# Performance work log

Measured on AMD Instinct MI355X. Metric: run time of the kernel, lower is better.

## Reference

```python
import jax, jax.numpy as jnp
import numpy as np

B_SZ, SEQ, D_IN = 8, 4096, 1024
STATE, HEADS = 1024, 16
HEAD_DIM = STATE // HEADS
LN_EPS = 1e-5


def setup_inputs() -> dict:
    key = jax.random.key(0)
    ks = jax.random.split(key, 10)
    inp = {
        "x": jax.random.normal(ks[0], (B_SZ, SEQ, D_IN), dtype=jnp.float32),
        "W_in": jax.random.normal(ks[1], (STATE, D_IN), dtype=jnp.float32) * (1.0 / np.sqrt(D_IN)),
        "b_in": jnp.zeros((STATE,), dtype=jnp.float32),
        "log_A": jax.random.normal(ks[2], (HEADS, HEAD_DIM), dtype=jnp.float32) * 0.1 + 0.1,
        "B_p": jax.random.normal(ks[3], (HEADS, HEAD_DIM), dtype=jnp.float32) * 0.1 + 0.1,
        "C_p": jax.random.normal(ks[4], (HEADS, HEAD_DIM), dtype=jnp.float32) * 0.1 + 0.1,
        "W_out": jax.random.normal(ks[5], (STATE, STATE), dtype=jnp.float32) * (1.0 / np.sqrt(STATE)),
        "b_out": jnp.zeros((STATE,), dtype=jnp.float32),
        "gamma": jnp.ones((STATE,), dtype=jnp.float32),
        "beta": jnp.zeros((STATE,), dtype=jnp.float32),
    }
    return inp


def reference(x, W_in, b_in, log_A, B_p, C_p, W_out, b_out, gamma, beta):
    Bsz, S, _ = x.shape
    H, Dh = log_A.shape
    # input projection: (B,S,state)
    h = jnp.einsum("bsd,ed->bse", x, W_in) + b_in
    h = h.reshape(Bsz, S, H, Dh)
    decay = jnp.exp(-jax.nn.softplus(log_A))  # (H,Dh), time-invariant

    def step(s, xt):  # s,xt: (B,H,Dh)
        s = s * decay + B_p * xt
        return s, C_p * s

    s0 = jnp.zeros((Bsz, H, Dh), dtype=h.dtype)
    _, ys = jax.lax.scan(step, s0, jnp.swapaxes(h, 0, 1))  # ys: (S,B,H,Dh)
    y = jnp.swapaxes(ys, 0, 1).reshape(Bsz, S, H * Dh)
    out = jnp.einsum("bse,fe->bsf", y, W_out) + b_out
    # dropout in eval mode = identity; layer norm over last dim
    mu = out.mean(-1, keepdims=True)
    var = out.var(-1, keepdims=True)
    return (out - mu) * jax.lax.rsqrt(var + LN_EPS) * gamma + beta
```

## Files before the change

### kernel.cpp

```cpp
#include <hip/hip_runtime.h>

#define B_SZ  8
#define SEQ   4096
#define D_IN  1024
#define STATE 1024
#define M_TOT (B_SZ * SEQ)
#define LN_EPS 1e-5f
#define GK    1024
#define GN    1024

#define SCAN_L 64
#define SCAN_W 64

typedef short short8_t __attribute__((ext_vector_type(8)));
typedef float f32x4 __attribute__((ext_vector_type(4)));

__device__ __forceinline__ unsigned short f2bf(float f) {
  union { float f; unsigned u; } v; v.f = f;
  unsigned r = v.u + 0x7fffu + ((v.u >> 16) & 1u);
  return (unsigned short)(r >> 16);
}
__device__ __forceinline__ float bf2f(unsigned short h) {
  union { unsigned u; float f; } v; v.u = ((unsigned)h) << 16;
  return v.f;
}

__device__ __forceinline__ void gload16(const void* g, void* l) {
  __builtin_amdgcn_global_load_lds(
      (const __attribute__((address_space(1))) void*)g,
      (__attribute__((address_space(3))) void*)l, 16, 0, 0);
}

#define BAR()    __builtin_amdgcn_s_barrier()
#define SCHED0() __builtin_amdgcn_sched_barrier(0)

__global__ __launch_bounds__(256) void cast_kernel(const float* __restrict__ in,
                                                   unsigned short* __restrict__ out,
                                                   int n4) {
  const int stride = gridDim.x * 256;
  for (int i = blockIdx.x * 256 + threadIdx.x; i < n4; i += stride) {
    float4 v = ((const float4*)in)[i];
    ushort4 o;
    o.x = f2bf(v.x); o.y = f2bf(v.y); o.z = f2bf(v.z); o.w = f2bf(v.w);
    ((ushort4*)out)[i] = o;
  }
}

__global__ __launch_bounds__(256) void cast2_kernel(const float* __restrict__ a,
                                                    const float* __restrict__ b,
                                                    unsigned short* __restrict__ oa,
                                                    unsigned short* __restrict__ ob,
                                                    int n4each) {
  const int stride = gridDim.x * 256;
  for (int i = blockIdx.x * 256 + threadIdx.x; i < 2 * n4each; i += stride) {
    const bool second = (i >= n4each);
    const int j = second ? i - n4each : i;
    float4 v = second ? ((const float4*)b)[j] : ((const float4*)a)[j];
    ushort4 o;
    o.x = f2bf(v.x); o.y = f2bf(v.y); o.z = f2bf(v.z); o.w = f2bf(v.w);
    if (second) ((ushort4*)ob)[j] = o; else ((ushort4*)oa)[j] = o;
  }
}

__device__ __forceinline__ void stageA(const char* g, char* d, int t) {
  gload16(g + t * 64, d);
}
__device__ __forceinline__ void stageB(const char* g, char* d, int t, int h) {
  gload16(g + h * (128 * (long)GK * 2) + t * 64, d + h * 8192);
}

template <int H>
__device__ __forceinline__ void readA(const char* pk, short8_t (&a)[2]) {
#pragma unroll
  for (int mf = 0; mf < 2; mf++)
    a[mf] = *(const short8_t*)(pk + H * 2048 + mf * 1024);
}
template <int NH>
__device__ __forceinline__ void readB(const char* pk, short8_t (&b)[2]) {
#pragma unroll
  for (int nf = 0; nf < 2; nf++)
    b[nf] = *(const short8_t*)(pk + NH * 2048 + nf * 1024);
}

template <int H, int NH>
__device__ __forceinline__ void mfma4(short8_t (&a)[2], short8_t (&b)[2],
                                      f32x4 (&acc)[4][4]) {
  __builtin_amdgcn_s_setprio(1);
#pragma unroll
  for (int mf = 0; mf < 2; mf++)
#pragma unroll
    for (int nf = 0; nf < 2; nf++)
      acc[H * 2 + mf][NH * 2 + nf] = __builtin_amdgcn_mfma_f32_16x16x32_bf16(
          a[mf], b[nf], acc[H * 2 + mf][NH * 2 + nf], 0, 0, 0);
  __builtin_amdgcn_s_setprio(0);
}

__global__ __launch_bounds__(512, 4) void gemm128(
    const unsigned short* __restrict__ A,
    const unsigned short* __restrict__ Bt,
    const float* __restrict__ bias,
    unsigned short* __restrict__ C,
    int M) {
  __shared__ __attribute__((aligned(16))) unsigned short As[2][128 * 32];
  __shared__ __attribute__((aligned(16))) unsigned short Bs[2][256 * 32];

  const int tid = threadIdx.x;
  const int w = tid >> 6, lane = tid & 63;
  const int wm = w >> 2, wn = w & 3;
  const int fr = lane & 15;
  const int fkb = (lane >> 4) * 16;

  const int nwg = gridDim.x;
  const int cpx = nwg >> 3;
  const int bid = blockIdx.x;
  const int wg = (bid & 7) * cpx + (bid >> 3);
  const int nbx = GN >> 8;
  const long m0 = (long)(wg / nbx) * 128;
  const long n0 = (long)(wg % nbx) * 256;

  const int ko = fkb ^ (((fr >> 1) & 3) << 4);
  const int rb = fr * 64 + ko;
  const char* pA0 = (const char*)&As[0][0] + wm * 4096 + rb;
  const char* pA1 = (const char*)&As[1][0] + wm * 4096 + rb;
  const char* pB0 = (const char*)&Bs[0][0] + wn * 4096 + rb;
  const char* pB1 = (const char*)&Bs[1][0] + wn * 4096 + rb;

  const int srow = tid >> 2;
  const int c2 = ((tid & 3) * 16) ^ (((srow >> 1) & 3) << 4);
  const char* gA0 = (const char*)(A  + (m0 + srow) * (long)GK) + c2;
  const char* gB0 = (const char*)(Bt + (n0 + srow) * (long)GK) + c2;
  char* dA0 = (char*)&As[0][0] + ((tid >> 6) << 10);
  char* dA1 = (char*)&As[1][0] + ((tid >> 6) << 10);
  char* dB0 = (char*)&Bs[0][0] + ((tid >> 6) << 10);
  char* dB1 = (char*)&Bs[1][0] + ((tid >> 6) << 10);

  short8_t aE[2], aO[2], b0[2], b1[2];
  f32x4 acc[4][4] = {};

  const int nit = (GK / 32) >> 1;

  stageA(gA0, dA0, 0);
  stageB(gB0, dB0, 0, 0);
  stageB(gB0, dB0, 0, 1);
  SCHED0();
  asm volatile("s_waitcnt vmcnt(0)" ::: "memory");
  BAR();

#pragma unroll 1
  for (int i = 0; i < nit; ++i) {
    const bool last = (i == nit - 1);
    const int t1 = 2 * i + 1, t2 = 2 * i + 2;

    readA<0>(pA0, aE);
    readB<0>(pB0, b0);
    stageA(gA0, dA1, t1);
    SCHED0(); BAR();
    mfma4<0, 0>(aE, b0, acc);
    SCHED0(); BAR();

    readB<1>(pB0, b1);
    stageB(gB0, dB1, t1, 0);
    stageB(gB0, dB1, t1, 1);
    SCHED0(); BAR();
    mfma4<0, 1>(aE, b1, acc);
    SCHED0(); BAR();

    readA<1>(pA0, aO);
    SCHED0(); BAR();
    mfma4<1, 0>(aO, b0, acc);
    SCHED0(); BAR();

    SCHED0(); BAR();
    mfma4<1, 1>(aO, b1, acc);
    SCHED0();
    asm volatile("s_waitcnt vmcnt(0)" ::: "memory");
    BAR();

    readA<0>(pA1, aE);
    readB<0>(pB1, b0);
    if (!last) stageA(gA0, dA0, t2);
    SCHED0(); BAR();
    mfma4<0, 0>(aE, b0, acc);
    SCHED0(); BAR();

    readB<1>(pB1, b1);
    if (!last) {
      stageB(gB0, dB0, t2, 0);
      stageB(gB0, dB0, t2, 1);
    }
    SCHED0(); BAR();
    mfma4<0, 1>(aE, b1, acc);
    SCHED0(); BAR();

    readA<1>(pA1, aO);
    SCHED0(); BAR();
    mfma4<1, 0>(aO, b0, acc);
    SCHED0(); BAR();

    SCHED0(); BAR();
    mfma4<1, 1>(aO, b1, acc);
    SCHED0();
    if (!last) { asm volatile("s_waitcnt vmcnt(0)" ::: "memory"); }
    BAR();
  }

  const int cc = lane & 15;
  const int cr = (lane >> 4) * 4;
  char* epi = (w < 4) ? ((char*)&As[0][0] + w * 4096)
                      : ((char*)&Bs[0][0] + (w - 4) * 4096);
  float bv[4];
#pragma unroll
  for (int nf = 0; nf < 4; nf++) bv[nf] = bias[n0 + wn * 64 + nf * 16 + cc];
  const int rr = lane >> 3;
  const int rdo = rr * 128 + (((lane & 7) * 16) ^ ((rr & 7) << 4));
#pragma unroll
  for (int half = 0; half < 2; ++half) {
#pragma unroll
    for (int m2 = 0; m2 < 2; ++m2) {
      const int mf = half * 2 + m2;
#pragma unroll
      for (int r = 0; r < 4; ++r) {
        const int rowc = m2 * 16 + cr + r;
        const int rx = (rowc & 7) << 4;
#pragma unroll
        for (int nf = 0; nf < 4; ++nf) {
          const int off = rowc * 128 + (((nf * 16 + cc) * 2) ^ rx);
          *(unsigned short*)(epi + off) = f2bf(acc[mf][nf][r] + bv[nf]);
        }
      }
    }
    char* cb = (char*)C + (m0 + wm * 64 + half * 32) * (GN * 2)
             + (n0 + wn * 64) * 2 + (lane & 7) * 16;
#pragma unroll
    for (int s = 0; s < 4; ++s) {
      short8_t vv = *(const short8_t*)(epi + s * 1024 + rdo);
      *(short8_t*)(cb + (long)(s * 8 + rr) * (GN * 2)) = vv;
    }
  }
}

__global__ __launch_bounds__(256) void scan_kernel(
    const unsigned short* __restrict__ h,
    const float* __restrict__ log_A,
    const float* __restrict__ Bp,
    const float* __restrict__ Cp,
    unsigned short* __restrict__ y) {
  const int e0 = threadIdx.x * 4;
  const int chunk = blockIdx.x;
  const int b = blockIdx.y;
  const float4 la = *(const float4*)&log_A[e0];
  const float4 bp = *(const float4*)&Bp[e0];
  const float4 cp = *(const float4*)&Cp[e0];
  float d[4], bpv[4], cpv[4];
  d[0] = expf(-log1pf(expf(la.x))); d[1] = expf(-log1pf(expf(la.y)));
  d[2] = expf(-log1pf(expf(la.z))); d[3] = expf(-log1pf(expf(la.w)));
  bpv[0] = bp.x; bpv[1] = bp.y; bpv[2] = bp.z; bpv[3] = bp.w;
  cpv[0] = cp.x; cpv[1] = cp.y; cpv[2] = cp.z; cpv[3] = cp.w;

  const long base = ((long)b * SEQ) * STATE + e0;
  const int t0 = chunk * SCAN_L;
  const int tw = (t0 >= SCAN_W) ? (t0 - SCAN_W) : 0;
  float s[4] = {0.f, 0.f, 0.f, 0.f};

  for (int t = tw; t < t0; ++t) {
    ushort4 hv = *(const ushort4*)&h[base + (long)t * STATE];
    s[0] = fmaf(s[0], d[0], bpv[0] * bf2f(hv.x));
    s[1] = fmaf(s[1], d[1], bpv[1] * bf2f(hv.y));
    s[2] = fmaf(s[2], d[2], bpv[2] * bf2f(hv.z));
    s[3] = fmaf(s[3], d[3], bpv[3] * bf2f(hv.w));
  }
  for (int t = t0; t < t0 + SCAN_L; ++t) {
    ushort4 hv = *(const ushort4*)&h[base + (long)t * STATE];
    s[0] = fmaf(s[0], d[0], bpv[0] * bf2f(hv.x));
    s[1] = fmaf(s[1], d[1], bpv[1] * bf2f(hv.y));
    s[2] = fmaf(s[2], d[2], bpv[2] * bf2f(hv.z));
    s[3] = fmaf(s[3], d[3], bpv[3] * bf2f(hv.w));
    ushort4 o;
    o.x = f2bf(cpv[0] * s[0]); o.y = f2bf(cpv[1] * s[1]);
    o.z = f2bf(cpv[2] * s[2]); o.w = f2bf(cpv[3] * s[3]);
    *(ushort4*)&y[base + (long)t * STATE] = o;
  }
}

__global__ __launch_bounds__(128) void ln_kernel(
    const unsigned short* __restrict__ X,
    const float* __restrict__ gamma,
    const float* __restrict__ beta,
    float* __restrict__ out) {
  const int row = blockIdx.x;
  const int tid = threadIdx.x;
  const long base = (long)row * STATE;
  short8_t v = *(const short8_t*)&X[base + tid * 8];
  float x[8];
#pragma unroll
  for (int j = 0; j < 8; j++) x[j] = bf2f((unsigned short)v[j]);
  float s = 0.f, q = 0.f;
#pragma unroll
  for (int j = 0; j < 8; j++) { s += x[j]; q += x[j] * x[j]; }
#pragma unroll
  for (int o = 32; o > 0; o >>= 1) {
    s += __shfl_xor(s, o);
    q += __shfl_xor(q, o);
  }
  __shared__ float sw[2], qw[2];
  const int wave = tid >> 6, lane = tid & 63;
  if (lane == 0) { sw[wave] = s; qw[wave] = q; }
  __syncthreads();
  s = sw[0] + sw[1];
  q = qw[0] + qw[1];
  const float mu = s * (1.0f / STATE);
  const float var = q * (1.0f / STATE) - mu * mu;
  const float inv = rsqrtf(var + LN_EPS);
  const int c = tid * 8;
  float4 g0 = *(const float4*)&gamma[c], g1 = *(const float4*)&gamma[c + 4];
  float4 be0 = *(const float4*)&beta[c], be1 = *(const float4*)&beta[c + 4];
  float4 o0, o1;
  o0.x = (x[0] - mu) * inv * g0.x + be0.x;
  o0.y = (x[1] - mu) * inv * g0.y + be0.y;
  o0.z = (x[2] - mu) * inv * g0.z + be0.z;
  o0.w = (x[3] - mu) * inv * g0.w + be0.w;
  o1.x = (x[4] - mu) * inv * g1.x + be1.x;
  o1.y = (x[5] - mu) * inv * g1.y + be1.y;
  o1.z = (x[6] - mu) * inv * g1.z + be1.z;
  o1.w = (x[7] - mu) * inv * g1.w + be1.w;
  *(float4*)&out[base + c] = o0;
  *(float4*)&out[base + c + 4] = o1;
}

extern "C" void kernel_launch(void* const* d_in, const int* in_sizes, int n_in,
                              void* d_out, int out_size, void* d_ws, size_t ws_size,
                              hipStream_t stream) {
  const float* x     = (const float*)d_in[0];
  const float* W_in  = (const float*)d_in[1];
  const float* b_in  = (const float*)d_in[2];
  const float* log_A = (const float*)d_in[3];
  const float* Bp    = (const float*)d_in[4];
  const float* Cp    = (const float*)d_in[5];
  const float* W_out = (const float*)d_in[6];
  const float* b_out = (const float*)d_in[7];
  const float* gamma = (const float*)d_in[8];
  const float* beta  = (const float*)d_in[9];
  float* out = (float*)d_out;

  char* ws = (char*)d_ws;
  unsigned short* Wi_b = (unsigned short*)(ws);
  unsigned short* Wo_b = (unsigned short*)(ws + (2ull << 20));
  unsigned short* xb   = (unsigned short*)(ws + (4ull << 20));
  unsigned short* hb   = (unsigned short*)(ws + (68ull << 20));

  cast_kernel<<<4096, 256, 0, stream>>>(x, xb, M_TOT * D_IN / 4);
  cast2_kernel<<<2048, 256, 0, stream>>>(W_in, W_out, Wi_b, Wo_b, STATE * D_IN / 4);

  gemm128<<<dim3((GN / 256) * (M_TOT / 128)), 512, 0, stream>>>(
      xb, Wi_b, b_in, hb, M_TOT);

  scan_kernel<<<dim3(SEQ / SCAN_L, B_SZ), 256, 0, stream>>>(
      hb, log_A, Bp, Cp, xb);

  gemm128<<<dim3((GN / 256) * (M_TOT / 128)), 512, 0, stream>>>(
      xb, Wo_b, b_out, hb, M_TOT);

  ln_kernel<<<M_TOT, 128, 0, stream>>>(hb, gamma, beta, out);
}
```

Measured before the change: 256.7 us.

## Fuse fp32-to-bf16 cast of x into the input-projection GEMM

Removes the standalone cast kernel for x and adds a GEMM variant that stages fp32 x tiles straight into LDS, converting them to bf16 when reading MFMA fragments. This avoids writing and re-reading the 64MB bf16 copy of x. In exchange the A tile in LDS doubles to fp32, which raises LDS use per block and may reduce occupancy, and every fragment read now does extra conversion work.

```diff
diff --git a/kernel.cpp b/kernel.cpp
--- a/kernel.cpp
+++ b/kernel.cpp
@@ -1,4 +1,5 @@
 #include <hip/hip_runtime.h>
+#include <hip/hip_bf16.h>
 
 #define B_SZ  8
 #define SEQ   4096
@@ -33,18 +34,6 @@
 
 #define BAR()    __builtin_amdgcn_s_barrier()
 #define SCHED0() __builtin_amdgcn_sched_barrier(0)
-
-__global__ __launch_bounds__(256) void cast_kernel(const float* __restrict__ in,
-                                                   unsigned short* __restrict__ out,
-                                                   int n4) {
-  const int stride = gridDim.x * 256;
-  for (int i = blockIdx.x * 256 + threadIdx.x; i < n4; i += stride) {
-    float4 v = ((const float4*)in)[i];
-    ushort4 o;
-    o.x = f2bf(v.x); o.y = f2bf(v.y); o.z = f2bf(v.z); o.w = f2bf(v.w);
-    ((ushort4*)out)[i] = o;
-  }
-}
 
 __global__ __launch_bounds__(256) void cast2_kernel(const float* __restrict__ a,
                                                     const float* __restrict__ b,
@@ -62,11 +51,8 @@
   }
 }
 
-__device__ __forceinline__ void stageA(const char* g, char* d, int t) {
-  gload16(g + t * 64, d);
-}
-__device__ __forceinline__ void stageB(const char* g, char* d, int t, int h) {
-  gload16(g + h * (128 * (long)GK * 2) + t * 64, d + h * 8192);
+__device__ __forceinline__ void stageT(const char* g, char* d, long gofs, int dofs) {
+  gload16(g + gofs, d + dofs);
 }
 
 template <int H>
@@ -80,6 +66,21 @@
 #pragma unroll
   for (int nf = 0; nf < 2; nf++)
     b[nf] = *(const short8_t*)(pk + NH * 2048 + nf * 1024);
+}
+template <int H>
+__device__ __forceinline__ void readAf(const char* pk, int koa, int kob,
+                                       short8_t (&a)[2]) {
+#pragma unroll
+  for (int mf = 0; mf < 2; mf++) {
+    f32x4 lo = *(const f32x4*)(pk + H * 4096 + mf * 2048 + koa);
+    f32x4 hi = *(const f32x4*)(pk + H * 4096 + mf * 2048 + kob);
+    union { __hip_bfloat16 h[8]; short8_t s8; } u;
+    u.h[0] = __float2bfloat16(lo[0]); u.h[1] = __float2bfloat16(lo[1]);
+    u.h[2] = __float2bfloat16(lo[2]); u.h[3] = __float2bfloat16(lo[3]);
+    u.h[4] = __float2bfloat16(hi[0]); u.h[5] = __float2bfloat16(hi[1]);
+    u.h[6] = __float2bfloat16(hi[2]); u.h[7] = __float2bfloat16(hi[3]);
+    a[mf] = u.s8;
+  }
 }
 
 template <int H, int NH>
@@ -93,6 +94,43 @@
       acc[H * 2 + mf][NH * 2 + nf] = __builtin_amdgcn_mfma_f32_16x16x32_bf16(
           a[mf], b[nf], acc[H * 2 + mf][NH * 2 + nf], 0, 0, 0);
   __builtin_amdgcn_s_setprio(0);
+}
+
+__device__ __forceinline__ void epilogue(f32x4 (&acc)[4][4], char* epi,
+                                         const float* bias, unsigned short* C,
+                                         long m0, long n0, int wm, int wn,
+                                         int lane) {
+  const int cc = lane & 15;
+  const int cr = (lane >> 4) * 4;
+  float bv[4];
+#pragma unroll
+  for (int nf = 0; nf < 4; nf++) bv[nf] = bias[n0 + wn * 64 + nf * 16 + cc];
+  const int rr = lane >> 3;
+  const int rdo = rr * 128 + (((lane & 7) * 16) ^ ((rr & 7) << 4));
+#pragma unroll
+  for (int half = 0; half < 2; ++half) {
+#pragma unroll
+    for (int m2 = 0; m2 < 2; ++m2) {
+      const int mf = half * 2 + m2;
+#pragma unroll
+      for (int r = 0; r < 4; ++r) {
+        const int rowc = m2 * 16 + cr + r;
+        const int rx = (rowc & 7) << 4;
+#pragma unroll
+        for (int nf = 0; nf < 4; ++nf) {
+          const int off = rowc * 128 + (((nf * 16 + cc) * 2) ^ rx);
+          *(unsigned short*)(epi + off) = f2bf(acc[mf][nf][r] + bv[nf]);
+        }
+      }
+    }
+    char* cb = (char*)C + (m0 + wm * 64 + half * 32) * (GN * 2)
+             + (n0 + wn * 64) * 2 + (lane & 7) * 16;
+#pragma unroll
+    for (int s = 0; s < 4; ++s) {
+      short8_t vv = *(const short8_t*)(epi + s * 1024 + rdo);
+      *(short8_t*)(cb + (long)(s * 8 + rr) * (GN * 2)) = vv;
+    }
+  }
 }
 
 __global__ __launch_bounds__(512, 4) void gemm128(
@@ -136,12 +174,12 @@
 
   short8_t aE[2], aO[2], b0[2], b1[2];
   f32x4 acc[4][4] = {};
-
   const int nit = (GK / 32) >> 1;
-
-  stageA(gA0, dA0, 0);
-  stageB(gB0, dB0, 0, 0);
-  stageB(gB0, dB0, 0, 1);
+  const long BH = 128 * (long)GK * 2;
+
+  stageT(gA0, dA0, 0, 0);
+  stageT(gB0, dB0, 0, 0);
+  stageT(gB0, dB0, BH, 8192);
   SCHED0();
   asm volatile("s_waitcnt vmcnt(0)" ::: "memory");
   BAR();
@@ -153,14 +191,14 @@
 
     readA<0>(pA0, aE);
     readB<0>(pB0, b0);
-    stageA(gA0, dA1, t1);
+    stageT(gA0, dA1, t1 * 64, 0);
     SCHED0(); BAR();
     mfma4<0, 0>(aE, b0, acc);
     SCHED0(); BAR();
 
     readB<1>(pB0, b1);
-    stageB(gB0, dB1, t1, 0);
-    stageB(gB0, dB1, t1, 1);
+    stageT(gB0, dB1, t1 * 64, 0);
+    stageT(gB0, dB1, BH + t1 * 64, 8192);
     SCHED0(); BAR();
     mfma4<0, 1>(aE, b1, acc);
     SCHED0(); BAR();
@@ -178,15 +216,15 @@
 
     readA<0>(pA1, aE);
     readB<0>(pB1, b0);
-    if (!last) stageA(gA0, dA0, t2);
+    if (!last) stageT(gA0, dA0, t2 * 64, 0);
     SCHED0(); BAR();
     mfma4<0, 0>(aE, b0, acc);
     SCHED0(); BAR();
 
     readB<1>(pB1, b1);
     if (!last) {
-      stageB(gB0, dB0, t2, 0);
-      stageB(gB0, dB0, t2, 1);
+      stageT(gB0, dB0, t2 * 64, 0);
+      stageT(gB0, dB0, BH + t2 * 64, 8192);
     }
     SCHED0(); BAR();
     mfma4<0, 1>(aE, b1, acc);
@@ -204,39 +242,135 @@
     BAR();
   }
 
-  const int cc = lane & 15;
-  const int cr = (lane >> 4) * 4;
   char* epi = (w < 4) ? ((char*)&As[0][0] + w * 4096)
                       : ((char*)&Bs[0][0] + (w - 4) * 4096);
-  float bv[4];
-#pragma unroll
-  for (int nf = 0; nf < 4; nf++) bv[nf] = bias[n0 + wn * 64 + nf * 16 + cc];
-  const int rr = lane >> 3;
-  const int rdo = rr * 128 + (((lane & 7) * 16) ^ ((rr & 7) << 4));
-#pragma unroll
-  for (int half = 0; half < 2; ++half) {
-#pragma unroll
-    for (int m2 = 0; m2 < 2; ++m2) {
-      const int mf = half * 2 + m2;
-#pragma unroll
-      for (int r = 0; r < 4; ++r) {
-        const int rowc = m2 * 16 + cr + r;
-        const int rx = (rowc & 7) << 4;
-#pragma unroll
-        for (int nf = 0; nf < 4; ++nf) {
-          const int off = rowc * 128 + (((nf * 16 + cc) * 2) ^ rx);
-          *(unsigned short*)(epi + off) = f2bf(acc[mf][nf][r] + bv[nf]);
-        }
-      }
+  epilogue(acc, epi, bias, C, m0, n0, wm, wn, lane);
+}
+
+__global__ __launch_bounds__(512, 4) void gemm128_xf32(
+    const float* __restrict__ X,
+    const unsigned short* __restrict__ Bt,
+    const float* __restrict__ bias,
+    unsigned short* __restrict__ C,
+    int M) {
+  __shared__ __attribute__((aligned(16))) float Af[2][128 * 32];
+  __shared__ __attribute__((aligned(16))) unsigned short Bs[2][256 * 32];
+
+  const int tid = threadIdx.x;
+  const int w = tid >> 6, lane = tid & 63;
+  const int wm = w >> 2, wn = w & 3;
+  const int fr = lane & 15;
+  const int fkb = (lane >> 4) * 16;
+  const int fkb4 = (lane >> 4) * 32;
+
+  const int nwg = gridDim.x;
+  const int cpx = nwg >> 3;
+  const int bid = blockIdx.x;
+  const int wg = (bid & 7) * cpx + (bid >> 3);
+  const int nbx = GN >> 8;
+  const long m0 = (long)(wg / nbx) * 128;
+  const long n0 = (long)(wg % nbx) * 256;
+
+  const int koB = fkb ^ (((fr >> 1) & 3) << 4);
+  const char* pB0 = (const char*)&Bs[0][0] + wn * 4096 + fr * 64 + koB;
+  const char* pB1 = (const char*)&Bs[1][0] + wn * 4096 + fr * 64 + koB;
+  const int xorv8 = (fr & 7) << 4;
+  const int koa = (fkb4 + 0)  ^ xorv8;
+  const int kob = (fkb4 + 16) ^ xorv8;
+  const char* pAf0 = (const char*)&Af[0][0] + (wm * 64 + fr) * 128;
+  const char* pAf1 = (const char*)&Af[1][0] + (wm * 64 + fr) * 128;
+
+  const int srA = tid >> 3;
+  const int c2A = ((tid & 7) * 16) ^ ((srA & 7) << 4);
+  const char* gAf = (const char*)(X + (m0 + srA) * (long)GK) + c2A;
+  const long AQ1 = 64 * (long)GK * 4;
+  const int srB = tid >> 2;
+  const int c2B = ((tid & 3) * 16) ^ (((srB >> 1) & 3) << 4);
+  const char* gB0 = (const char*)(Bt + (n0 + srB) * (long)GK) + c2B;
+  const long BH = 128 * (long)GK * 2;
+
+  char* dAf0 = (char*)&Af[0][0] + ((tid >> 6) << 10);
+  char* dAf1 = (char*)&Af[1][0] + ((tid >> 6) << 10);
+  char* dB0 = (char*)&Bs[0][0] + ((tid >> 6) << 10);
+  char* dB1 = (char*)&Bs[1][0] + ((tid >> 6) << 10);
+
+  short8_t aE[2], aO[2], b0[2], b1[2];
+  f32x4 acc[4][4] = {};
+  const int nit = (GK / 32) >> 1;
+
+  stageT(gAf, dAf0, 0, 0);
+  stageT(gAf, dAf0, AQ1, 8192);
+  stageT(gB0, dB0, 0, 0);
+  stageT(gB0, dB0, BH, 8192);
+  SCHED0();
+  asm volatile("s_waitcnt vmcnt(0)" ::: "memory");
+  BAR();
+
+#pragma unroll 1
+  for (int i = 0; i < nit; ++i) {
+    const bool last = (i == nit - 1);
+    const int t1 = 2 * i + 1, t2 = 2 * i + 2;
+
+    readAf<0>(pAf0, koa, kob, aE);
+    readB<0>(pB0, b0);
+    stageT(gAf, dAf1, (long)t1 * 128, 0);
+    stageT(gAf, dAf1, AQ1 + (long)t1 * 128, 8192);
+    SCHED0(); BAR();
+    mfma4<0, 0>(aE, b0, acc);
+    SCHED0(); BAR();
+
+    readB<1>(pB0, b1);
+    stageT(gB0, dB1, t1 * 64, 0);
+    stageT(gB0, dB1, BH + t1 * 64, 8192);
+    SCHED0(); BAR();
+    mfma4<0, 1>(aE, b1, acc);
+    SCHED0(); BAR();
+
+    readAf<1>(pAf0, koa, kob, aO);
+    SCHED0(); BAR();
+    mfma4<1, 0>(aO, b0, acc);
+    SCHED0(); BAR();
+
+    SCHED0(); BAR();
+    mfma4<1, 1>(aO, b1, acc);
+    SCHED0();
+    asm volatile("s_waitcnt vmcnt(0)" ::: "memory");
+    BAR();
+
+    readAf<0>(pAf1, koa, kob, aE);
+    readB<0>(pB1, b0);
+    if (!last) {
+      stageT(gAf, dAf0, (long)t2 * 128, 0);
+      stageT(gAf, dAf0, AQ1 + (long)t2 * 128, 8192);
     }
-    char* cb = (char*)C + (m0 + wm * 64 + half * 32) * (GN * 2)
-             + (n0 + wn * 64) * 2 + (lane & 7) * 16;
-#pragma unroll
-    for (int s = 0; s < 4; ++s) {
-      short8_t vv = *(const short8_t*)(epi + s * 1024 + rdo);
-      *(short8_t*)(cb + (long)(s * 8 + rr) * (GN * 2)) = vv;
+    SCHED0(); BAR();
+    mfma4<0, 0>(aE, b0, acc);
+    SCHED0(); BAR();
+
+    readB<1>(pB1, b1);
+    if (!last) {
+      stageT(gB0, dB0, t2 * 64, 0);
+      stageT(gB0, dB0, BH + t2 * 64, 8192);
     }
-  }
+    SCHED0(); BAR();
+    mfma4<0, 1>(aE, b1, acc);
+    SCHED0(); BAR();
+
+    readAf<1>(pAf1, koa, kob, aO);
+    SCHED0(); BAR();
+    mfma4<1, 0>(aO, b0, acc);
+    SCHED0(); BAR();
+
+    SCHED0(); BAR();
+    mfma4<1, 1>(aO, b1, acc);
+    SCHED0();
+    if (!last) { asm volatile("s_waitcnt vmcnt(0)" ::: "memory"); }
+    BAR();
+  }
+
+  char* epi = (w < 4) ? ((char*)&Af[0][0] + w * 4096)
+                      : ((char*)&Bs[0][0] + (w - 4) * 4096);
+  epilogue(acc, epi, bias, C, m0, n0, wm, wn, lane);
 }
 
 __global__ __launch_bounds__(256) void scan_kernel(
@@ -345,20 +479,19 @@
   char* ws = (char*)d_ws;
   unsigned short* Wi_b = (unsigned short*)(ws);
   unsigned short* Wo_b = (unsigned short*)(ws + (2ull << 20));
-  unsigned short* xb   = (unsigned short*)(ws + (4ull << 20));
+  unsigned short* yb   = (unsigned short*)(ws + (4ull << 20));
   unsigned short* hb   = (unsigned short*)(ws + (68ull << 20));
 
-  cast_kernel<<<4096, 256, 0, stream>>>(x, xb, M_TOT * D_IN / 4);
   cast2_kernel<<<2048, 256, 0, stream>>>(W_in, W_out, Wi_b, Wo_b, STATE * D_IN / 4);
 
+  gemm128_xf32<<<dim3((GN / 256) * (M_TOT / 128)), 512, 0, stream>>>(
+      x, Wi_b, b_in, hb, M_TOT);
+
+  scan_kernel<<<dim3(SEQ / SCAN_L, B_SZ), 256, 0, stream>>>(
+      hb, log_A, Bp, Cp, yb);
+
   gemm128<<<dim3((GN / 256) * (M_TOT / 128)), 512, 0, stream>>>(
-      xb, Wi_b, b_in, hb, M_TOT);
-
-  scan_kernel<<<dim3(SEQ / SCAN_L, B_SZ), 256, 0, stream>>>(
-      hb, log_A, Bp, Cp, xb);
-
-  gemm128<<<dim3((GN / 256) * (M_TOT / 128)), 512, 0, stream>>>(
-      xb, Wo_b, b_out, hb, M_TOT);
+      yb, Wo_b, b_out, hb, M_TOT);
 
   ln_kernel<<<M_TOT, 128, 0, stream>>>(hb, gamma, beta, out);
 }
```

New measurement: 263.2 us. 1.03x slower.
